# Kernel tuning notes

Measured on AMD Instinct MI355X. Metric: run time of the kernel, lower is better.

Reference implementation:

```python
import jax, jax.numpy as jnp
import numpy as np
from jax import lax

EPS_LN = 1e-5
EPS_NORM = 1e-12
NUM_HEADS = 8
KV_HEADS = 2
REP = NUM_HEADS // KV_HEADS


def _layernorm_c(x, w, b):
    # WithBias LayerNorm over channel dim; x: [b,c,h,w]
    mu = x.mean(axis=1, keepdims=True)
    var = ((x - mu) ** 2).mean(axis=1, keepdims=True)
    return (x - mu) / jnp.sqrt(var + EPS_LN) * w[None, :, None, None] + b[None, :, None, None]


def _conv1x1(x, w):
    # x: [b,c,h,w], w: [o,c]
    return jnp.einsum('bchw,oc->bohw', x, w)


def _dwconv3x3(x, w):
    # depthwise 3x3, SAME padding; w: [C,1,3,3]
    C = x.shape[1]
    return lax.conv_general_dilated(
        x, w, window_strides=(1, 1), padding='SAME',
        dimension_numbers=('NCHW', 'OIHW', 'NCHW'), feature_group_count=C)


def _l2norm(x):
    # normalize over last axis (torch F.normalize semantics)
    n = jnp.sqrt(jnp.sum(x * x, axis=-1, keepdims=True))
    return x / jnp.maximum(n, EPS_NORM)


def setup_inputs() -> dict:
    key = jax.random.key(0)
    ks = jax.random.split(key, 8)
    b, dim, h, w = 4, 192, 256, 256
    kv_ch = 2 * dim // REP  # 96
    return {
        'x': jax.random.normal(ks[0], (b, dim, h, w), jnp.float32),
        'ln_w': jnp.ones((dim,), jnp.float32),
        'ln_b': jnp.zeros((dim,), jnp.float32),
        'q_w': jax.random.normal(ks[1], (dim, dim), jnp.float32) * 0.02,
        'q_dw': jax.random.normal(ks[2], (dim, 1, 3, 3), jnp.float32) * 0.1,
        'kv_w': jax.random.normal(ks[3], (kv_ch, dim), jnp.float32) * 0.02,
        'kv_dw': jax.random.normal(ks[4], (kv_ch, 1, 3, 3), jnp.float32) * 0.1,
        'proj_w': jax.random.normal(ks[5], (dim, dim), jnp.float32) * 0.02,
        'temperature': jnp.ones((NUM_HEADS, 1, 1), jnp.float32),
    }


def reference(x, ln_w, ln_b, q_w, q_dw, kv_w, kv_dw, proj_w, temperature):
    b, c, h, w = x.shape
    xn = _layernorm_c(x, ln_w, ln_b)
    q = _dwconv3x3(_conv1x1(xn, q_w), q_dw)            # [b, c, h, w]
    kv = _dwconv3x3(_conv1x1(xn, kv_w), kv_dw)         # [b, 2c/rep, h, w]
    k, v = jnp.split(kv, 2, axis=1)
    hw = h * w
    ch = c // NUM_HEADS
    q = q.reshape(b, NUM_HEADS, ch, hw)
    k = k.reshape(b, KV_HEADS, ch, hw)
    v = v.reshape(b, KV_HEADS, ch, hw)
    k = jnp.repeat(k, REP, axis=1)                     # repeat_kv
    v = jnp.repeat(v, REP, axis=1)
    q = _l2norm(q)
    k = _l2norm(k)
    attn = jnp.einsum('bhcn,bhdn->bhcd', q, k) * temperature[None]
    attn = jax.nn.softmax(attn, axis=-1)
    out = jnp.einsum('bhcd,bhdn->bhcn', attn, v)
    out = out.reshape(b, c, h, w)
    return _conv1x1(out, proj_w)
```

## Files before the change

### kernel.cpp

```cpp
#include <hip/hip_runtime.h>
#include <hip/hip_bf16.h>
#include <stdint.h>

#define HW    65536
#define NB    4
#define CIN   192
#define OYC   288
#define BSTR  200
#define EPS   72

__device__ __forceinline__ float bflo(unsigned u){ return __uint_as_float(u << 16); }
__device__ __forceinline__ float bfhi(unsigned u){ return __uint_as_float(u & 0xffff0000u); }
__device__ __forceinline__ float bf2f(__hip_bfloat16 v){ return __bfloat162float(v); }
__device__ __forceinline__ unsigned short f2bfbits(float f){
  __hip_bfloat16 h = __float2bfloat16(f); return *(unsigned short*)&h;
}

__device__ __forceinline__ void unpack8(uint4 u, float* f) {
  f[0]=bflo(u.x); f[1]=bfhi(u.x); f[2]=bflo(u.y); f[3]=bfhi(u.y);
  f[4]=bflo(u.z); f[5]=bfhi(u.z); f[6]=bflo(u.w); f[7]=bfhi(u.w);
}

union BF8 { uint4 u; __hip_bfloat16 h[8]; };

typedef __attribute__((ext_vector_type(8))) short short8;
typedef __attribute__((ext_vector_type(4))) float floatx4;

__global__ void k_prep(const float* __restrict__ qw, const float* __restrict__ kvw,
                       const float* __restrict__ lnw, const float* __restrict__ lnb,
                       __hip_bfloat16* __restrict__ AF, float* __restrict__ bias) {
  int blk = blockIdx.x, t = threadIdx.x;
  if (blk < 32) {
    for (int i = blk * 256 + t; i < OYC * CIN; i += 32 * 256) {
      int o = i / CIN, c = i % CIN;
      float w = (o < 192) ? qw[o * 192 + c] : kvw[(o - 192) * 192 + c];
      float val = w * lnw[c];
      int ot = o >> 4, lo = o & 15;
      int ks = c >> 5, cr = c & 31, q = cr >> 3, j = cr & 7;
      int dst = (((ot * 6 + ks) * 64) + q * 16 + lo) * 8 + j;
      AF[dst] = __float2bfloat16(val);
    }
  } else {
    for (int o = t; o < OYC; o += 256) {
      float s = 0.f;
      for (int c = 0; c < CIN; ++c)
        s += ((o < 192) ? qw[o * 192 + c] : kvw[(o - 192) * 192 + c]) * lnb[c];
      bias[o] = s;
    }
  }
}

__global__ __launch_bounds__(256, 4) void k_conv1(const float* __restrict__ x,
                                                  const __hip_bfloat16* __restrict__ AF,
                                                  const float* __restrict__ bias,
                                                  __hip_bfloat16* __restrict__ y) {
  __shared__ __align__(16) __hip_bfloat16 Bl[64 * BSTR];
  __shared__ float part[4][64][2];
  __shared__ float murs[64][2];
  __shared__ float biasl[OYC];
  int bid = blockIdx.x;
  int b  = bid >> 10;
  int n0 = (bid & 1023) * 64;
  int tid = threadIdx.x;
  int p = tid & 63, g = tid >> 6;

  for (int i = tid; i < OYC; i += 256) biasl[i] = bias[i];

  const float* xb = x + (size_t)(b * CIN + g * 48) * HW + n0 + p;
  float xv[48];
  float s = 0.f, ss = 0.f;
#pragma unroll
  for (int j = 0; j < 48; ++j) {
    float v = xb[(size_t)j * HW];
    xv[j] = v; s += v; ss += v * v;
  }
  part[g][p][0] = s; part[g][p][1] = ss;
  __syncthreads();
  if (tid < 64) {
    float s0 = 0.f, s1 = 0.f;
#pragma unroll
    for (int gg = 0; gg < 4; ++gg) { s0 += part[gg][tid][0]; s1 += part[gg][tid][1]; }
    float m = s0 * (1.f / CIN);
    float var = s1 * (1.f / CIN) - m * m;
    murs[tid][0] = m; murs[tid][1] = rsqrtf(var + 1e-5f);
  }
  __syncthreads();
  float mu = murs[p][0], rs = murs[p][1];
#pragma unroll
  for (int j = 0; j < 48; j += 2) {
    unsigned lo = f2bfbits((xv[j]     - mu) * rs);
    unsigned hi = f2bfbits((xv[j + 1] - mu) * rs);
    *(unsigned*)&Bl[p * BSTR + g * 48 + j] = lo | (hi << 16);
  }
  __syncthreads();

  int wave = tid >> 6, lane = tid & 63;
  int wo = wave >> 1, wn = wave & 1;
  int li = lane & 15, q = lane >> 4;

  floatx4 acc[9][2];
#pragma unroll
  for (int t = 0; t < 9; ++t)
#pragma unroll
    for (int nt = 0; nt < 2; ++nt) acc[t][nt] = (floatx4){0.f, 0.f, 0.f, 0.f};

  const __hip_bfloat16* abase = AF + ((size_t)(wo * 9) * 6 * 64 + lane) * 8;
  short8 a0[9], a1[9];
#pragma unroll
  for (int t = 0; t < 9; ++t) a0[t] = *(const short8*)(abase + (size_t)(t * 6) * 512);

#pragma unroll
  for (int ks = 0; ks < 6; ++ks) {
    short8 bf0 = *(const short8*)&Bl[(wn * 32 + li) * BSTR + ks * 32 + q * 8];
    short8 bf1 = *(const short8*)&Bl[(wn * 32 + 16 + li) * BSTR + ks * 32 + q * 8];
    if (ks < 5) {
#pragma unroll
      for (int t = 0; t < 9; ++t) {
        short8 v = *(const short8*)(abase + (size_t)(t * 6 + ks + 1) * 512);
        if (ks & 1) a0[t] = v; else a1[t] = v;
      }
    }
#pragma unroll
    for (int t = 0; t < 9; ++t) {
      short8 af = (ks & 1) ? a1[t] : a0[t];
      acc[t][0] = __builtin_amdgcn_mfma_f32_16x16x32_bf16(af, bf0, acc[t][0], 0, 0, 0);
      acc[t][1] = __builtin_amdgcn_mfma_f32_16x16x32_bf16(af, bf1, acc[t][1], 0, 0, 0);
    }
  }

  __hip_bfloat16* EP = Bl;
  int row = tid >> 3, cg8 = (tid & 7) * 8;
#pragma unroll
  for (int ph = 0; ph < 2; ++ph) {
    __syncthreads();
    if (wo == ph) {
#pragma unroll
      for (int t = 0; t < 9; ++t)
#pragma unroll
        for (int nt = 0; nt < 2; ++nt)
#pragma unroll
          for (int r = 0; r < 4; ++r) {
            int orow = t * 16 + q * 4 + r;
            int pp = wn * 32 + nt * 16 + li;
            EP[orow * EPS + pp] = __float2bfloat16(acc[t][nt][r] + biasl[ph * 144 + orow]);
          }
    }
    __syncthreads();
#pragma unroll
    for (int it = 0; it < 5; ++it) {
      int rr = it * 32 + row;
      if (rr < 144) {
        uint4 u = *(const uint4*)&EP[rr * EPS + cg8];
        *(uint4*)&y[(size_t)(b * OYC + ph * 144 + rr) * HW + n0 + cg8] = u;
      }
    }
  }
}

__global__ __launch_bounds__(256) void k_dwkv(const __hip_bfloat16* __restrict__ y,
                                              const float* __restrict__ kvdw,
                                              __hip_bfloat16* __restrict__ kbuf,
                                              __hip_bfloat16* __restrict__ vbuf,
                                              float* __restrict__ kss) {
  __shared__ __align__(16) __hip_bfloat16 stage[18 * 256];
  int bid = blockIdx.x;
  int hb = bid & 15;
  int ck = (bid >> 4) % 96;
  int b  = bid / (16 * 96);
  int tid = threadIdx.x;
  int h0 = hb * 16;

  const __hip_bfloat16* yp = y + (size_t)(b * OYC + 192 + ck) * HW;
  for (int i = tid; i < 18 * 32; i += 256) {
    int ry = i >> 5, seg = i & 31;
    int hh = h0 - 1 + ry;
    uint4 u = make_uint4(0u, 0u, 0u, 0u);
    if ((unsigned)hh < 256u) u = *(const uint4*)(yp + hh * 256 + seg * 8);
    *(uint4*)&stage[ry * 256 + seg * 8] = u;
  }
  __syncthreads();

  float w[9];
#pragma unroll
  for (int i = 0; i < 9; ++i) w[i] = kvdw[ck * 9 + i];

  int cg = tid & 31, rg = tid >> 5;
  int c0 = cg * 8;
  bool isk = (ck < 48);
  __hip_bfloat16* ob = (isk ? kbuf : vbuf) + (size_t)(b * 48 + (ck % 48)) * HW;
  float ssq = 0.f;
#pragma unroll
  for (int rr = 0; rr < 2; ++rr) {
    int orow = rg * 2 + rr;
    float o[8];
#pragma unroll
    for (int j = 0; j < 8; ++j) o[j] = 0.f;
#pragma unroll
    for (int ry = 0; ry < 3; ++ry) {
      const __hip_bfloat16* rb = &stage[(orow + ry) * 256];
      float v[8];
      unpack8(*(const uint4*)&rb[c0], v);
      float vl = (c0 > 0)       ? bf2f(rb[c0 - 1]) : 0.f;
      float vr = (c0 + 8 < 256) ? bf2f(rb[c0 + 8]) : 0.f;
      float wl = w[ry * 3], wm = w[ry * 3 + 1], wr = w[ry * 3 + 2];
      o[0] = fmaf(wl, vl, fmaf(wm, v[0], fmaf(wr, v[1], o[0])));
#pragma unroll
      for (int j = 1; j < 7; ++j)
        o[j] = fmaf(wl, v[j-1], fmaf(wm, v[j], fmaf(wr, v[j+1], o[j])));
      o[7] = fmaf(wl, v[6], fmaf(wm, v[7], fmaf(wr, vr, o[7])));
    }
    BF8 t;
#pragma unroll
    for (int j = 0; j < 8; ++j) {
      t.h[j] = __float2bfloat16(o[j]);
      if (isk) { float fv = bf2f(t.h[j]); ssq += fv * fv; }
    }
    *(uint4*)(ob + (size_t)(h0 + orow) * 256 + c0) = t.u;
  }
  if (isk) {
#pragma unroll
    for (int off = 32; off > 0; off >>= 1) ssq += __shfl_down(ssq, off);
    __shared__ float ws4[4];
    if ((tid & 63) == 0) ws4[tid >> 6] = ssq;
    __syncthreads();
    if (tid == 0) atomicAdd(&kss[b * 48 + ck], ws4[0] + ws4[1] + ws4[2] + ws4[3]);
  }
}

__global__ __launch_bounds__(256) void k_dwq(const __hip_bfloat16* __restrict__ y,
                                             const float* __restrict__ qdw,
                                             __hip_bfloat16* __restrict__ qfull,
                                             float* __restrict__ qss) {
  __shared__ __align__(16) __hip_bfloat16 stage[18 * 256];
  int bid = blockIdx.x;
  int hb = bid & 15;
  int c  = (bid >> 4) % 192;
  int b  = bid / (16 * 192);
  int tid = threadIdx.x;
  int h0 = hb * 16;

  const __hip_bfloat16* yp = y + (size_t)(b * OYC + c) * HW;
  for (int i = tid; i < 18 * 32; i += 256) {
    int ry = i >> 5, seg = i & 31;
    int hh = h0 - 1 + ry;
    uint4 u = make_uint4(0u, 0u, 0u, 0u);
    if ((unsigned)hh < 256u) u = *(const uint4*)(yp + hh * 256 + seg * 8);
    *(uint4*)&stage[ry * 256 + seg * 8] = u;
  }
  __syncthreads();

  float w[9];
#pragma unroll
  for (int i = 0; i < 9; ++i) w[i] = qdw[c * 9 + i];

  int cg = tid & 31, rg = tid >> 5;
  int c0 = cg * 8;
  __hip_bfloat16* ob = qfull + (size_t)(b * CIN + c) * HW;
  float ssq = 0.f;
#pragma unroll
  for (int rr = 0; rr < 2; ++rr) {
    int orow = rg * 2 + rr;
    float o[8];
#pragma unroll
    for (int j = 0; j < 8; ++j) o[j] = 0.f;
#pragma unroll
    for (int ry = 0; ry < 3; ++ry) {
      const __hip_bfloat16* rb = &stage[(orow + ry) * 256];
      float v[8];
      unpack8(*(const uint4*)&rb[c0], v);
      float vl = (c0 > 0)       ? bf2f(rb[c0 - 1]) : 0.f;
      float vr = (c0 + 8 < 256) ? bf2f(rb[c0 + 8]) : 0.f;
      float wl = w[ry * 3], wm = w[ry * 3 + 1], wr = w[ry * 3 + 2];
      o[0] = fmaf(wl, vl, fmaf(wm, v[0], fmaf(wr, v[1], o[0])));
#pragma unroll
      for (int j = 1; j < 7; ++j)
        o[j] = fmaf(wl, v[j-1], fmaf(wm, v[j], fmaf(wr, v[j+1], o[j])));
      o[7] = fmaf(wl, v[6], fmaf(wm, v[7], fmaf(wr, vr, o[7])));
    }
    BF8 t;
#pragma unroll
    for (int j = 0; j < 8; ++j) {
      t.h[j] = __float2bfloat16(o[j]);
      float fv = bf2f(t.h[j]); ssq += fv * fv;
    }
    *(uint4*)(ob + (size_t)(h0 + orow) * 256 + c0) = t.u;
  }
#pragma unroll
  for (int off = 32; off > 0; off >>= 1) ssq += __shfl_down(ssq, off);
  __shared__ float ws4[4];
  if ((tid & 63) == 0) ws4[tid >> 6] = ssq;
  __syncthreads();
  if (tid == 0) atomicAdd(&qss[b * 192 + c], ws4[0] + ws4[1] + ws4[2] + ws4[3]);
}

__global__ __launch_bounds__(256) void k_qk(const __hip_bfloat16* __restrict__ qfull,
                                            const __hip_bfloat16* __restrict__ kbuf,
                                            float* __restrict__ attn) {
  __shared__ float red[96 * 33];
  int bid = blockIdx.x;
  int ck  = bid & 63;
  int kvh = (bid >> 6) & 1;
  int b   = bid >> 7;
  int tid = threadIdx.x;
  int wave = tid >> 6, lane = tid & 63;
  int li = lane & 15, qd = lane >> 4;

  for (int i = tid; i < 96 * 33; i += 256) red[i] = 0.f;

  const __hip_bfloat16* qp = qfull + (size_t)(b * CIN + kvh * 96) * HW;
  const __hip_bfloat16* kp = kbuf  + (size_t)(b * 48 + kvh * 24) * HW;
  int n0 = ck * 1024 + wave * 256;

  floatx4 acc[6][2];
#pragma unroll
  for (int mt = 0; mt < 6; ++mt) {
    acc[mt][0] = (floatx4){0.f, 0.f, 0.f, 0.f};
    acc[mt][1] = (floatx4){0.f, 0.f, 0.f, 0.f};
  }

  int kr1 = 16 + li; if (kr1 > 23) kr1 = 23;
  for (int ks = 0; ks < 8; ++ks) {
    int nn = n0 + ks * 32 + qd * 8;
    short8 bk0 = *(const short8*)(kp + (size_t)li  * HW + nn);
    short8 bk1 = *(const short8*)(kp + (size_t)kr1 * HW + nn);
#pragma unroll
    for (int mt = 0; mt < 6; ++mt) {
      short8 aq = *(const short8*)(qp + (size_t)(mt * 16 + li) * HW + nn);
      acc[mt][0] = __builtin_amdgcn_mfma_f32_16x16x32_bf16(aq, bk0, acc[mt][0], 0, 0, 0);
      acc[mt][1] = __builtin_amdgcn_mfma_f32_16x16x32_bf16(aq, bk1, acc[mt][1], 0, 0, 0);
    }
  }
  __syncthreads();

#pragma unroll
  for (int mt = 0; mt < 6; ++mt) {
#pragma unroll
    for (int nt = 0; nt < 2; ++nt) {
      int n = nt * 16 + li;
      if (n < 24) {
#pragma unroll
        for (int r = 0; r < 4; ++r) {
          int m = mt * 16 + qd * 4 + r;
          atomicAdd(&red[m * 33 + n], acc[mt][nt][r]);
        }
      }
    }
  }
  __syncthreads();

  for (int i = tid; i < 96 * 24; i += 256) {
    int m = i / 24, d = i % 24;
    int head = kvh * 4 + m / 24, cp = m % 24;
    atomicAdd(&attn[(((b * 8 + head) * 24) + cp) * 24 + d], red[m * 33 + d]);
  }
}

__global__ void k_attn_final(const float* __restrict__ attn, const float* __restrict__ qss,
                             const float* __restrict__ kss, const float* __restrict__ temp,
                             const float* __restrict__ projw, float* __restrict__ Mt) {
  int b = blockIdx.x;
  int t = threadIdx.x;
  __shared__ float as_[96 * 25];
  float acc[48];
#pragma unroll
  for (int j = 0; j < 48; ++j) acc[j] = 0.f;
  for (int kvh = 0; kvh < 2; ++kvh) {
    __syncthreads();
    if (t < 96) {
      int row = kvh * 96 + t;
      int h = row / 24, cp = row % 24;
      float rq = 1.f / fmaxf(sqrtf(qss[b * 192 + row]), 1e-12f);
      float tp = temp[h];
      float lg[24]; float mx = -1e30f;
#pragma unroll
      for (int d = 0; d < 24; ++d) {
        float rk = 1.f / fmaxf(sqrtf(kss[b * 48 + kvh * 24 + d]), 1e-12f);
        float l = attn[(((b * 8 + h) * 24) + cp) * 24 + d] * rq * rk * tp;
        lg[d] = l; mx = fmaxf(mx, l);
      }
      float s = 0.f;
#pragma unroll
      for (int d = 0; d < 24; ++d) { lg[d] = __expf(lg[d] - mx); s += lg[d]; }
      float inv = 1.f / s;
#pragma unroll
      for (int d = 0; d < 24; ++d) as_[t * 25 + d] = lg[d] * inv;
    }
    __syncthreads();
    if (t < 192) {
      for (int cc = 0; cc < 96; ++cc) {
        float pw = projw[t * 192 + kvh * 96 + cc];
        const float* ar = &as_[cc * 25];
#pragma unroll
        for (int d = 0; d < 24; ++d) acc[kvh * 24 + d] = fmaf(pw, ar[d], acc[kvh * 24 + d]);
      }
    }
  }
  if (t < 192) {
#pragma unroll
    for (int j = 0; j < 48; ++j) Mt[((size_t)b * 48 + j) * 192 + t] = acc[j];
  }
}

__global__ __launch_bounds__(256) void k_out(const __hip_bfloat16* __restrict__ vbuf,
                                             const float* __restrict__ Mt,
                                             float* __restrict__ out) {
  __shared__ __align__(16) __hip_bfloat16 lv[48 * 256];
  int bid = blockIdx.x;
  int b  = bid >> 8;
  int n0 = (bid & 255) * 256;
  int tid = threadIdx.x;
  const __hip_bfloat16* vb = vbuf + (size_t)b * 48 * HW + n0;
  for (int i = tid; i < 48 * 32; i += 256) {
    int c = i >> 5, seg = i & 31;
    *(uint4*)&lv[c * 256 + seg * 8] = *(const uint4*)(vb + (size_t)c * HW + seg * 8);
  }
  __syncthreads();
  int wave = tid >> 6, ln = tid & 63;
  const float* mb = Mt + (size_t)b * 48 * 192;
  for (int ch = 0; ch < 2; ++ch) {
    int o0 = wave * 48 + ch * 24;
    float acc[24][4];
#pragma unroll
    for (int j = 0; j < 24; ++j)
#pragma unroll
      for (int e = 0; e < 4; ++e) acc[j][e] = 0.f;
    for (int c = 0; c < 48; ++c) {
      float xv[4];
      uint2 u = *(const uint2*)&lv[c * 256 + ln * 4];
      xv[0] = bflo(u.x); xv[1] = bfhi(u.x); xv[2] = bflo(u.y); xv[3] = bfhi(u.y);
      const float* mrow = mb + c * 192 + o0;
      float4 m[6];
#pragma unroll
      for (int gg = 0; gg < 6; ++gg) m[gg] = *(const float4*)(mrow + gg * 4);
      const float* mf = (const float*)&m[0];
#pragma unroll
      for (int j = 0; j < 24; ++j) {
        float mv = mf[j];
#pragma unroll
        for (int e = 0; e < 4; ++e) acc[j][e] = fmaf(mv, xv[e], acc[j][e]);
      }
    }
#pragma unroll
    for (int j = 0; j < 24; ++j) {
      float4 st = make_float4(acc[j][0], acc[j][1], acc[j][2], acc[j][3]);
      *(float4*)&out[(size_t)(b * 192 + o0 + j) * HW + n0 + ln * 4] = st;
    }
  }
}

extern "C" void kernel_launch(void* const* d_in, const int* in_sizes, int n_in,
                              void* d_out, int out_size, void* d_ws, size_t ws_size,
                              hipStream_t stream) {
  const float* x     = (const float*)d_in[0];
  const float* ln_w  = (const float*)d_in[1];
  const float* ln_b  = (const float*)d_in[2];
  const float* q_w   = (const float*)d_in[3];
  const float* q_dw  = (const float*)d_in[4];
  const float* kv_w  = (const float*)d_in[5];
  const float* kv_dw = (const float*)d_in[6];
  const float* projw = (const float*)d_in[7];
  const float* temp  = (const float*)d_in[8];
  float* out = (float*)d_out;
  float* wsf = (float*)d_ws;

  float* qss  = wsf;
  float* kss  = wsf + 768;
  float* attn = wsf + 960;
  float* Mt   = wsf + 19392;
  float* bias = wsf + 56256;
  __hip_bfloat16* AF = (__hip_bfloat16*)(wsf + 56544);
  __hip_bfloat16* y    = (__hip_bfloat16*)(wsf + 111872);
  __hip_bfloat16* kbuf = (__hip_bfloat16*)(wsf + 37860608);
  __hip_bfloat16* vbuf = (__hip_bfloat16*)(wsf + 44152064);
  __hip_bfloat16* qfull = (__hip_bfloat16*)d_out;

  hipMemsetAsync(wsf, 0, 19392 * sizeof(float), stream);
  hipLaunchKernelGGL(k_prep, dim3(33), dim3(256), 0, stream, q_w, kv_w, ln_w, ln_b, AF, bias);
  hipLaunchKernelGGL(k_conv1, dim3(NB * 1024), dim3(256), 0, stream, x, AF, bias, y);
  hipLaunchKernelGGL(k_dwkv, dim3(NB * 96 * 16), dim3(256), 0, stream, y, kv_dw, kbuf, vbuf, kss);
  hipLaunchKernelGGL(k_dwq, dim3(NB * 192 * 16), dim3(256), 0, stream, y, q_dw, qfull, qss);
  hipLaunchKernelGGL(k_qk, dim3(NB * 2 * 64), dim3(256), 0, stream, qfull, kbuf, attn);
  hipLaunchKernelGGL(k_attn_final, dim3(NB), dim3(256), 0, stream, attn, qss, kss, temp, projw, Mt);
  hipLaunchKernelGGL(k_out, dim3(NB * 256), dim3(256), 0, stream, vbuf, Mt, out);
}
```

Measured before the change: 664.3 us.

## Fold LayerNorm into conv1x1 epilogue and enlarge pixel tile per block

```diff
diff --git a/kernel.cpp b/kernel.cpp
--- a/kernel.cpp
+++ b/kernel.cpp
@@ -7,7 +7,7 @@
 #define CIN   192
 #define OYC   288
 #define BSTR  200
-#define EPS   72
+#define EPS2  264
 
 __device__ __forceinline__ float bflo(unsigned u){ return __uint_as_float(u << 16); }
 __device__ __forceinline__ float bfhi(unsigned u){ return __uint_as_float(u & 0xffff0000u); }
@@ -28,7 +28,8 @@
 
 __global__ void k_prep(const float* __restrict__ qw, const float* __restrict__ kvw,
                        const float* __restrict__ lnw, const float* __restrict__ lnb,
-                       __hip_bfloat16* __restrict__ AF, float* __restrict__ bias) {
+                       __hip_bfloat16* __restrict__ AF, float* __restrict__ bias,
+                       float* __restrict__ Ssum) {
   int blk = blockIdx.x, t = threadIdx.x;
   if (blk < 32) {
     for (int i = blk * 256 + t; i < OYC * CIN; i += 32 * 256) {
@@ -42,77 +43,91 @@
     }
   } else {
     for (int o = t; o < OYC; o += 256) {
-      float s = 0.f;
-      for (int c = 0; c < CIN; ++c)
-        s += ((o < 192) ? qw[o * 192 + c] : kvw[(o - 192) * 192 + c]) * lnb[c];
+      float s = 0.f, s2 = 0.f;
+      for (int c = 0; c < CIN; ++c) {
+        float w = (o < 192) ? qw[o * 192 + c] : kvw[(o - 192) * 192 + c];
+        s += w * lnb[c];
+        s2 += bf2f(__float2bfloat16(w * lnw[c]));
+      }
       bias[o] = s;
-    }
-  }
-}
-
-__global__ __launch_bounds__(256, 4) void k_conv1(const float* __restrict__ x,
-                                                  const __hip_bfloat16* __restrict__ AF,
-                                                  const float* __restrict__ bias,
-                                                  __hip_bfloat16* __restrict__ y) {
-  __shared__ __align__(16) __hip_bfloat16 Bl[64 * BSTR];
-  __shared__ float part[4][64][2];
-  __shared__ float murs[64][2];
+      Ssum[o] = s2;
+    }
+  }
+}
+
+__global__ __launch_bounds__(512, 2) void k_conv1r(const float* __restrict__ x,
+                                                   const __hip_bfloat16* __restrict__ AF,
+                                                   const float* __restrict__ bias,
+                                                   const float* __restrict__ Ssum,
+                                                   __hip_bfloat16* __restrict__ y) {
+  __shared__ __align__(16) __hip_bfloat16 Bl[256 * BSTR];
+  __shared__ float part_s[8][256];
+  __shared__ float part_q[8][256];
+  __shared__ float murs[256][2];
   __shared__ float biasl[OYC];
+  __shared__ float Sl[OYC];
+
   int bid = blockIdx.x;
-  int b  = bid >> 10;
-  int n0 = (bid & 1023) * 64;
+  int b = bid >> 8;
+  int r = bid & 255;
   int tid = threadIdx.x;
-  int p = tid & 63, g = tid >> 6;
-
-  for (int i = tid; i < OYC; i += 256) biasl[i] = bias[i];
-
-  const float* xb = x + (size_t)(b * CIN + g * 48) * HW + n0 + p;
-  float xv[48];
-  float s = 0.f, ss = 0.f;
-#pragma unroll
-  for (int j = 0; j < 48; ++j) {
-    float v = xb[(size_t)j * HW];
-    xv[j] = v; s += v; ss += v * v;
-  }
-  part[g][p][0] = s; part[g][p][1] = ss;
-  __syncthreads();
-  if (tid < 64) {
-    float s0 = 0.f, s1 = 0.f;
-#pragma unroll
-    for (int gg = 0; gg < 4; ++gg) { s0 += part[gg][tid][0]; s1 += part[gg][tid][1]; }
-    float m = s0 * (1.f / CIN);
-    float var = s1 * (1.f / CIN) - m * m;
-    murs[tid][0] = m; murs[tid][1] = rsqrtf(var + 1e-5f);
-  }
-  __syncthreads();
-  float mu = murs[p][0], rs = murs[p][1];
-#pragma unroll
-  for (int j = 0; j < 48; j += 2) {
-    unsigned lo = f2bfbits((xv[j]     - mu) * rs);
-    unsigned hi = f2bfbits((xv[j + 1] - mu) * rs);
-    *(unsigned*)&Bl[p * BSTR + g * 48 + j] = lo | (hi << 16);
-  }
-  __syncthreads();
-
-  int wave = tid >> 6, lane = tid & 63;
-  int wo = wave >> 1, wn = wave & 1;
-  int li = lane & 15, q = lane >> 4;
-
-  floatx4 acc[9][2];
+  int w = tid >> 6, l = tid & 63;
+
+  for (int i = tid; i < OYC; i += 512) { biasl[i] = bias[i]; Sl[i] = Ssum[i]; }
+
+  {
+    const float* xb = x + (size_t)(b * CIN + w * 24) * HW + r * 256 + l * 4;
+    float s[4] = {0.f, 0.f, 0.f, 0.f}, q2[4] = {0.f, 0.f, 0.f, 0.f};
+    unsigned pk[4][12];
+#pragma unroll
+    for (int c = 0; c < 24; ++c) {
+      float4 v4 = *(const float4*)(xb + (size_t)c * HW);
+      float vv[4] = {v4.x, v4.y, v4.z, v4.w};
+#pragma unroll
+      for (int i = 0; i < 4; ++i) {
+        s[i] += vv[i]; q2[i] += vv[i] * vv[i];
+        unsigned bits = f2bfbits(vv[i]);
+        if ((c & 1) == 0) pk[i][c >> 1] = bits;
+        else              pk[i][c >> 1] |= bits << 16;
+      }
+    }
+#pragma unroll
+    for (int i = 0; i < 4; ++i) {
+      int px = l * 4 + i;
+#pragma unroll
+      for (int j = 0; j < 3; ++j) {
+        uint4 u = make_uint4(pk[i][j*4], pk[i][j*4+1], pk[i][j*4+2], pk[i][j*4+3]);
+        *(uint4*)&Bl[px * BSTR + w * 24 + j * 8] = u;
+      }
+    }
+    *(float4*)&part_s[w][l * 4] = make_float4(s[0], s[1], s[2], s[3]);
+    *(float4*)&part_q[w][l * 4] = make_float4(q2[0], q2[1], q2[2], q2[3]);
+  }
+  __syncthreads();
+
+  int lane = tid & 63;
+  int mh = w >> 2, nq = w & 3;
+  int li = lane & 15, qd = lane >> 4;
+
+  floatx4 acc[9][4];
 #pragma unroll
   for (int t = 0; t < 9; ++t)
 #pragma unroll
-    for (int nt = 0; nt < 2; ++nt) acc[t][nt] = (floatx4){0.f, 0.f, 0.f, 0.f};
-
-  const __hip_bfloat16* abase = AF + ((size_t)(wo * 9) * 6 * 64 + lane) * 8;
+    for (int nt = 0; nt < 4; ++nt) acc[t][nt] = (floatx4){0.f, 0.f, 0.f, 0.f};
+
+  const __hip_bfloat16* abase = AF + ((size_t)(mh * 9) * 6 * 64 + lane) * 8;
   short8 a0[9], a1[9];
 #pragma unroll
   for (int t = 0; t < 9; ++t) a0[t] = *(const short8*)(abase + (size_t)(t * 6) * 512);
 
 #pragma unroll
   for (int ks = 0; ks < 6; ++ks) {
-    short8 bf0 = *(const short8*)&Bl[(wn * 32 + li) * BSTR + ks * 32 + q * 8];
-    short8 bf1 = *(const short8*)&Bl[(wn * 32 + 16 + li) * BSTR + ks * 32 + q * 8];
+    short8 bf[4];
+#pragma unroll
+    for (int nt = 0; nt < 4; ++nt) {
+      int px = nq * 64 + nt * 16 + li;
+      bf[nt] = *(const short8*)&Bl[px * BSTR + ks * 32 + qd * 8];
+    }
     if (ks < 5) {
 #pragma unroll
       for (int t = 0; t < 9; ++t) {
@@ -123,36 +138,46 @@
 #pragma unroll
     for (int t = 0; t < 9; ++t) {
       short8 af = (ks & 1) ? a1[t] : a0[t];
-      acc[t][0] = __builtin_amdgcn_mfma_f32_16x16x32_bf16(af, bf0, acc[t][0], 0, 0, 0);
-      acc[t][1] = __builtin_amdgcn_mfma_f32_16x16x32_bf16(af, bf1, acc[t][1], 0, 0, 0);
-    }
+#pragma unroll
+      for (int nt = 0; nt < 4; ++nt)
+        acc[t][nt] = __builtin_amdgcn_mfma_f32_16x16x32_bf16(af, bf[nt], acc[t][nt], 0, 0, 0);
+    }
+  }
+
+  if (tid < 256) {
+    float s0 = 0.f, s1 = 0.f;
+#pragma unroll
+    for (int g = 0; g < 8; ++g) { s0 += part_s[g][tid]; s1 += part_q[g][tid]; }
+    float m = s0 * (1.f / CIN);
+    float var = s1 * (1.f / CIN) - m * m;
+    murs[tid][0] = m;
+    murs[tid][1] = rsqrtf(var + 1e-5f);
   }
 
   __hip_bfloat16* EP = Bl;
-  int row = tid >> 3, cg8 = (tid & 7) * 8;
 #pragma unroll
   for (int ph = 0; ph < 2; ++ph) {
     __syncthreads();
-    if (wo == ph) {
+    if (mh == ph) {
 #pragma unroll
       for (int t = 0; t < 9; ++t)
 #pragma unroll
-        for (int nt = 0; nt < 2; ++nt)
-#pragma unroll
-          for (int r = 0; r < 4; ++r) {
-            int orow = t * 16 + q * 4 + r;
-            int pp = wn * 32 + nt * 16 + li;
-            EP[orow * EPS + pp] = __float2bfloat16(acc[t][nt][r] + biasl[ph * 144 + orow]);
+        for (int nt = 0; nt < 4; ++nt) {
+          int px = nq * 64 + nt * 16 + li;
+          float mu = murs[px][0], rs = murs[px][1];
+#pragma unroll
+          for (int rr = 0; rr < 4; ++rr) {
+            int ol = t * 16 + qd * 4 + rr;
+            float val = rs * (acc[t][nt][rr] - mu * Sl[ph * 144 + ol]) + biasl[ph * 144 + ol];
+            EP[ol * EPS2 + px] = __float2bfloat16(val);
           }
+        }
     }
     __syncthreads();
-#pragma unroll
-    for (int it = 0; it < 5; ++it) {
-      int rr = it * 32 + row;
-      if (rr < 144) {
-        uint4 u = *(const uint4*)&EP[rr * EPS + cg8];
-        *(uint4*)&y[(size_t)(b * OYC + ph * 144 + rr) * HW + n0 + cg8] = u;
-      }
+    for (int i = tid; i < 144 * 32; i += 512) {
+      int row = i >> 5, seg = i & 31;
+      uint4 u = *(const uint4*)&EP[row * EPS2 + seg * 8];
+      *(uint4*)&y[(size_t)(b * OYC + ph * 144 + row) * HW + r * 256 + seg * 8] = u;
     }
   }
 }
@@ -468,15 +493,16 @@
   float* attn = wsf + 960;
   float* Mt   = wsf + 19392;
   float* bias = wsf + 56256;
-  __hip_bfloat16* AF = (__hip_bfloat16*)(wsf + 56544);
+  float* Ssum = wsf + 56544;
+  __hip_bfloat16* AF = (__hip_bfloat16*)(wsf + 56832);
   __hip_bfloat16* y    = (__hip_bfloat16*)(wsf + 111872);
   __hip_bfloat16* kbuf = (__hip_bfloat16*)(wsf + 37860608);
   __hip_bfloat16* vbuf = (__hip_bfloat16*)(wsf + 44152064);
   __hip_bfloat16* qfull = (__hip_bfloat16*)d_out;
 
   hipMemsetAsync(wsf, 0, 19392 * sizeof(float), stream);
-  hipLaunchKernelGGL(k_prep, dim3(33), dim3(256), 0, stream, q_w, kv_w, ln_w, ln_b, AF, bias);
-  hipLaunchKernelGGL(k_conv1, dim3(NB * 1024), dim3(256), 0, stream, x, AF, bias, y);
+  hipLaunchKernelGGL(k_prep, dim3(33), dim3(256), 0, stream, q_w, kv_w, ln_w, ln_b, AF, bias, Ssum);
+  hipLaunchKernelGGL(k_conv1r, dim3(NB * 256), dim3(512), 0, stream, x, AF, bias, Ssum, y);
   hipLaunchKernelGGL(k_dwkv, dim3(NB * 96 * 16), dim3(256), 0, stream, y, kv_dw, kbuf, vbuf, kss);
   hipLaunchKernelGGL(k_dwq, dim3(NB * 192 * 16), dim3(256), 0, stream, y, q_dw, qfull, qss);
   hipLaunchKernelGGL(k_qk, dim3(NB * 2 * 64), dim3(256), 0, stream, qfull, kbuf, attn);
```

Measured after the change: 678.1 us. 1.02x slower.
